# Kernel tuning notes

Hardware: AMD Instinct MI355X
Metric: run time of the kernel (lower is better)

The kernel has to match this reference:

```python
import jax, jax.numpy as jnp
import numpy as np

S, B, H = 2048, 32, 1024

def setup_inputs() -> dict:
    key = jax.random.key(0)
    k1, k2, k3, k4, k5 = jax.random.split(key, 5)
    stdv = 1.0 / np.sqrt(2 * H)  # nn.Linear default init scale (approx, uniform in torch)
    return {
        "hidden": jax.random.normal(k1, (1, B, H), dtype=jnp.float32),
        "encoder_outputs": jax.random.normal(k2, (S, B, H), dtype=jnp.float32),
        "W": jax.random.normal(k3, (H, 2 * H), dtype=jnp.float32) * stdv,
        "b": jax.random.normal(k4, (H,), dtype=jnp.float32) * stdv,
        "v": jax.random.normal(k5, (H,), dtype=jnp.float32) * (1.0 / np.sqrt(H)),
    }

def reference(hidden, encoder_outputs, W, b, v):
    # hidden: (1, B, H); encoder_outputs: (S, B, H)
    h = hidden[0]                              # (B, H)
    e = jnp.swapaxes(encoder_outputs, 0, 1)    # (B, S, H)
    Wh, We = W[:, :H], W[:, H:]                # split concat-linear: cat([H_rep, enc]) @ W^T
    # energy = tanh(Linear(cat([H, enc], -1)))  -> (B, S, H)
    pre_h = h @ Wh.T                           # (B, H), broadcast over S (H is repeated per step)
    pre_e = jnp.einsum('bsh,kh->bsk', e, We)   # (B, S, H)
    energy = jnp.tanh(pre_e + pre_h[:, None, :] + b)
    scores = jnp.einsum('bsk,k->bs', energy, v)  # v-dot per position -> (B, S)
    return jax.nn.softmax(scores, axis=1)[:, None, :]  # (B, 1, S)
```

## Files before the change

### kernel.cpp

```cpp
#include <hip/hip_runtime.h>


#define LDT 40

typedef __attribute__((ext_vector_type(8))) short short8;
typedef __attribute__((ext_vector_type(4))) float floatx4;
typedef __attribute__((ext_vector_type(4))) unsigned int uint4v;

#define GLDS(g, l) __builtin_amdgcn_global_load_lds( \
    (const __attribute__((address_space(1))) void*)(g), \
    (__attribute__((address_space(3))) void*)(l), 16, 0, 0)

__device__ __forceinline__ unsigned short f2b(float f) {
  union { float f; unsigned u; } c; c.f = f;
  unsigned r = c.u + 0x7fffu + ((c.u >> 16) & 1u);
  return (unsigned short)(r >> 16);
}

__device__ __forceinline__ unsigned pack2(float lo, float hi) {
  union { float f; unsigned u; } a, b; a.f = lo; b.f = hi;
  return __builtin_amdgcn_perm(b.u + 0x8000u, a.u + 0x8000u, 0x07060302u);
}

__device__ __forceinline__ float fast_tanh(float x) {
  float e = __expf(2.0f * x);
  return 1.0f - 2.0f / (e + 1.0f);
}

__global__ __launch_bounds__(256) void k_cvtB(
    const float* __restrict__ W, unsigned int* __restrict__ Bw) {
  const int idx = blockIdx.x * 256 + threadIdx.x;
  const int row = idx >> 8, col = (idx & 255) << 2;
  float4 f = *(const float4*)(W + (size_t)row * 2048 + 1024 + col);
  unsigned u0 = (unsigned)f2b(f.x) | ((unsigned)f2b(f.y) << 16);
  unsigned u1 = (unsigned)f2b(f.z) | ((unsigned)f2b(f.w) << 16);
  uint2 u = {u0, u1};
  *(uint2*)(Bw + ((size_t)row * 1024 + col) / 2) = u;
}

__global__ __launch_bounds__(256) void k_preh(
    const float* __restrict__ hidden, const float* __restrict__ W,
    const float* __restrict__ bias, float* __restrict__ tpre) {
  const int wv   = (blockIdx.x << 2) + (threadIdx.x >> 6);
  const int lane = threadIdx.x & 63;
  const int b = wv & 31;
  const int k = wv >> 5;
  const float* wr = W + (size_t)k * 2048;
  const float* hr = hidden + b * 1024;
  float s = 0.f;
  #pragma unroll
  for (int j = 0; j < 1024; j += 64) s += wr[j + lane] * hr[j + lane];
  #pragma unroll
  for (int off = 32; off; off >>= 1) s += __shfl_xor(s, off, 64);
  if (lane == 0) tpre[b * 1024 + k] = s + bias[k];
}

__global__ __launch_bounds__(256) void k_gemm(
    const float* __restrict__ A,
    const unsigned short* __restrict__ Bw,
    const float* __restrict__ tpre,
    const float* __restrict__ vvec,
    float* __restrict__ scoresT) {
  __shared__ short As[128 * LDT];
  __shared__ short Bs[128 * 32];

  const int l = blockIdx.x;
  const int x = l & 7, j = l >> 3;
  const int Mbase = (x * 64 + (j >> 3)) * 128;
  const int Nbase = (j & 7) * 128;

  const int tid = threadIdx.x, lane = tid & 63, w = tid >> 6;
  const int wm = w >> 1, wn = w & 1;
  const int c = lane & 15, q = lane >> 4;

  const float* ap = A + (size_t)(Mbase + (tid >> 1)) * 1024 + ((tid & 1) << 4);
  short* asw = &As[(tid >> 1) * LDT + ((tid & 1) << 4)];

  const unsigned short* bg0 =
      Bw + (size_t)(Nbase + w * 32 + (lane >> 2)) * 1024 + ((lane & 3) << 3);
  const unsigned short* bg1 = bg0 + (size_t)16 * 1024;
  short* bl0 = &Bs[(w * 32) * 32];
  short* bl1 = &Bs[(w * 32 + 16) * 32];

  floatx4 acc[4][4];
  #pragma unroll
  for (int mt = 0; mt < 4; ++mt)
    #pragma unroll
    for (int nt = 0; nt < 4; ++nt) {
      floatx4 z = {0.f, 0.f, 0.f, 0.f};
      acc[mt][nt] = z;
    }

  for (int k0 = 0; k0 < 1024; k0 += 32) {
    float4 f0 = *(const float4*)(ap + k0);
    float4 f1 = *(const float4*)(ap + k0 + 4);
    float4 f2 = *(const float4*)(ap + k0 + 8);
    float4 f3 = *(const float4*)(ap + k0 + 12);
    __syncthreads();
    GLDS(bg0 + k0, bl0);
    GLDS(bg1 + k0, bl1);
    uint4v u0 = {pack2(f0.x, f0.y), pack2(f0.z, f0.w),
                 pack2(f1.x, f1.y), pack2(f1.z, f1.w)};
    uint4v u1 = {pack2(f2.x, f2.y), pack2(f2.z, f2.w),
                 pack2(f3.x, f3.y), pack2(f3.z, f3.w)};
    *(uint4v*)asw = u0;
    *(uint4v*)(asw + 8) = u1;
    __syncthreads();

    short8 af[4], bf[4];
    #pragma unroll
    for (int mt = 0; mt < 4; ++mt)
      af[mt] = *(const short8*)&As[(wm * 64 + mt * 16 + c) * LDT + q * 8];
    #pragma unroll
    for (int nt = 0; nt < 4; ++nt)
      bf[nt] = *(const short8*)&Bs[(wn * 64 + nt * 16 + c) * 32 + q * 8];
    #pragma unroll
    for (int mt = 0; mt < 4; ++mt)
      #pragma unroll
      for (int nt = 0; nt < 4; ++nt)
        acc[mt][nt] = __builtin_amdgcn_mfma_f32_16x16x32_bf16(
            af[mt], bf[nt], acc[mt][nt], 0, 0, 0);
  }

  const int mwave = Mbase + wm * 64;
  const int nwave = Nbase + wn * 64;
  float vv[4];
  #pragma unroll
  for (int nt = 0; nt < 4; ++nt) vv[nt] = vvec[nwave + nt * 16 + c];
  #pragma unroll
  for (int mt = 0; mt < 4; ++mt) {
    #pragma unroll
    for (int i = 0; i < 4; ++i) {
      const int mrow = mwave + mt * 16 + q * 4 + i;
      const float* tb = tpre + (mrow & 31) * 1024;
      float ssum = 0.f;
      #pragma unroll
      for (int nt = 0; nt < 4; ++nt) {
        float pre = acc[mt][nt][i] + tb[nwave + nt * 16 + c];
        ssum += fast_tanh(pre) * vv[nt];
      }
      #pragma unroll
      for (int off = 1; off < 16; off <<= 1) ssum += __shfl_xor(ssum, off, 64);
      if (c == 0) atomicAdd(&scoresT[(mrow & 31) * 2048 + (mrow >> 5)], ssum);
    }
  }
}

__global__ __launch_bounds__(256) void k_softmax(
    const float* __restrict__ scoresT, float* __restrict__ out) {
  const int b = blockIdx.x;
  const int t = threadIdx.x;
  const int w = t >> 6, lane = t & 63;
  __shared__ float red[4];
  float vals[8];
  float m = -3.0e38f;
  #pragma unroll
  for (int i = 0; i < 8; ++i) {
    vals[i] = scoresT[b * 2048 + t + 256 * i];
    m = fmaxf(m, vals[i]);
  }
  #pragma unroll
  for (int off = 32; off; off >>= 1) m = fmaxf(m, __shfl_xor(m, off, 64));
  if (lane == 0) red[w] = m;
  __syncthreads();
  m = fmaxf(fmaxf(red[0], red[1]), fmaxf(red[2], red[3]));
  __syncthreads();
  float e[8];
  float sum = 0.f;
  #pragma unroll
  for (int i = 0; i < 8; ++i) { e[i] = __expf(vals[i] - m); sum += e[i]; }
  #pragma unroll
  for (int off = 32; off; off >>= 1) sum += __shfl_xor(sum, off, 64);
  if (lane == 0) red[w] = sum;
  __syncthreads();
  sum = red[0] + red[1] + red[2] + red[3];
  const float inv = 1.0f / sum;
  #pragma unroll
  for (int i = 0; i < 8; ++i) out[b * 2048 + t + 256 * i] = e[i] * inv;
}

extern "C" void kernel_launch(void* const* d_in, const int* in_sizes, int n_in,
                              void* d_out, int out_size, void* d_ws, size_t ws_size,
                              hipStream_t stream) {
  const float* hidden = (const float*)d_in[0];
  const float* enc    = (const float*)d_in[1];
  const float* W      = (const float*)d_in[2];
  const float* bias   = (const float*)d_in[3];
  const float* vvec   = (const float*)d_in[4];
  float* out = (float*)d_out;

  float* scoresT = (float*)d_ws;
  float* tpre    = scoresT + 65536;
  unsigned int* Bw = (unsigned int*)(tpre + 32768);

  hipMemsetAsync(scoresT, 0, 65536 * sizeof(float), stream);
  hipLaunchKernelGGL(k_cvtB, dim3(1024), dim3(256), 0, stream, W, Bw);
  hipLaunchKernelGGL(k_preh, dim3(8192), dim3(256), 0, stream, hidden, W, bias, tpre);
  hipLaunchKernelGGL(k_gemm, dim3(4096), dim3(256), 0, stream,
                     enc, (const unsigned short*)Bw, tpre, vvec, scoresT);
  hipLaunchKernelGGL(k_softmax, dim3(32), dim3(256), 0, stream, scoresT, out);
}
```

Baseline: 719.5 us.

## Double-buffer GEMM LDS tiles and fold score zeroing into conversion kernel

```diff
diff --git a/kernel.cpp b/kernel.cpp
--- a/kernel.cpp
+++ b/kernel.cpp
@@ -28,7 +28,8 @@
 }
 
 __global__ __launch_bounds__(256) void k_cvtB(
-    const float* __restrict__ W, unsigned int* __restrict__ Bw) {
+    const float* __restrict__ W, unsigned int* __restrict__ Bw,
+    float* __restrict__ scoresT) {
   const int idx = blockIdx.x * 256 + threadIdx.x;
   const int row = idx >> 8, col = (idx & 255) << 2;
   float4 f = *(const float4*)(W + (size_t)row * 2048 + 1024 + col);
@@ -36,6 +37,7 @@
   unsigned u1 = (unsigned)f2b(f.z) | ((unsigned)f2b(f.w) << 16);
   uint2 u = {u0, u1};
   *(uint2*)(Bw + ((size_t)row * 1024 + col) / 2) = u;
+  if (blockIdx.x < 256) scoresT[blockIdx.x * 256 + threadIdx.x] = 0.f;
 }
 
 __global__ __launch_bounds__(256) void k_preh(
@@ -61,8 +63,8 @@
     const float* __restrict__ tpre,
     const float* __restrict__ vvec,
     float* __restrict__ scoresT) {
-  __shared__ short As[128 * LDT];
-  __shared__ short Bs[128 * 32];
+  __shared__ short As[2][128 * LDT];
+  __shared__ short Bs[2][128 * 32];
 
   const int l = blockIdx.x;
   const int x = l & 7, j = l >> 3;
@@ -73,14 +75,14 @@
   const int wm = w >> 1, wn = w & 1;
   const int c = lane & 15, q = lane >> 4;
 
+  const int aoff = (tid >> 1) * LDT + ((tid & 1) << 4);
   const float* ap = A + (size_t)(Mbase + (tid >> 1)) * 1024 + ((tid & 1) << 4);
-  short* asw = &As[(tid >> 1) * LDT + ((tid & 1) << 4)];
 
   const unsigned short* bg0 =
       Bw + (size_t)(Nbase + w * 32 + (lane >> 2)) * 1024 + ((lane & 3) << 3);
   const unsigned short* bg1 = bg0 + (size_t)16 * 1024;
-  short* bl0 = &Bs[(w * 32) * 32];
-  short* bl1 = &Bs[(w * 32 + 16) * 32];
+  const int boff0 = (w * 32) * 32;
+  const int boff1 = (w * 32 + 16) * 32;
 
   floatx4 acc[4][4];
   #pragma unroll
@@ -91,35 +93,60 @@
       acc[mt][nt] = z;
     }
 
-  for (int k0 = 0; k0 < 1024; k0 += 32) {
-    float4 f0 = *(const float4*)(ap + k0);
-    float4 f1 = *(const float4*)(ap + k0 + 4);
-    float4 f2 = *(const float4*)(ap + k0 + 8);
-    float4 f3 = *(const float4*)(ap + k0 + 12);
-    __syncthreads();
-    GLDS(bg0 + k0, bl0);
-    GLDS(bg1 + k0, bl1);
+  {
+    float4 f0 = *(const float4*)(ap);
+    float4 f1 = *(const float4*)(ap + 4);
+    float4 f2 = *(const float4*)(ap + 8);
+    float4 f3 = *(const float4*)(ap + 12);
+    GLDS(bg0, &Bs[0][boff0]);
+    GLDS(bg1, &Bs[0][boff1]);
     uint4v u0 = {pack2(f0.x, f0.y), pack2(f0.z, f0.w),
                  pack2(f1.x, f1.y), pack2(f1.z, f1.w)};
     uint4v u1 = {pack2(f2.x, f2.y), pack2(f2.z, f2.w),
                  pack2(f3.x, f3.y), pack2(f3.z, f3.w)};
-    *(uint4v*)asw = u0;
-    *(uint4v*)(asw + 8) = u1;
-    __syncthreads();
+    *(uint4v*)&As[0][aoff] = u0;
+    *(uint4v*)&As[0][aoff + 8] = u1;
+  }
+  __syncthreads();
+
+  for (int k0 = 0; k0 < 1024; k0 += 32) {
+    const int cur = (k0 >> 5) & 1;
+    const int nxt = cur ^ 1;
+    const bool more = (k0 + 32) < 1024;
+
+    float4 g0, g1, g2, g3;
+    if (more) {
+      g0 = *(const float4*)(ap + k0 + 32);
+      g1 = *(const float4*)(ap + k0 + 36);
+      g2 = *(const float4*)(ap + k0 + 40);
+      g3 = *(const float4*)(ap + k0 + 44);
+      GLDS(bg0 + k0 + 32, &Bs[nxt][boff0]);
+      GLDS(bg1 + k0 + 32, &Bs[nxt][boff1]);
+    }
 
     short8 af[4], bf[4];
     #pragma unroll
     for (int mt = 0; mt < 4; ++mt)
-      af[mt] = *(const short8*)&As[(wm * 64 + mt * 16 + c) * LDT + q * 8];
+      af[mt] = *(const short8*)&As[cur][(wm * 64 + mt * 16 + c) * LDT + q * 8];
     #pragma unroll
     for (int nt = 0; nt < 4; ++nt)
-      bf[nt] = *(const short8*)&Bs[(wn * 64 + nt * 16 + c) * 32 + q * 8];
+      bf[nt] = *(const short8*)&Bs[cur][(wn * 64 + nt * 16 + c) * 32 + q * 8];
     #pragma unroll
     for (int mt = 0; mt < 4; ++mt)
       #pragma unroll
       for (int nt = 0; nt < 4; ++nt)
         acc[mt][nt] = __builtin_amdgcn_mfma_f32_16x16x32_bf16(
             af[mt], bf[nt], acc[mt][nt], 0, 0, 0);
+
+    if (more) {
+      uint4v u0 = {pack2(g0.x, g0.y), pack2(g0.z, g0.w),
+                   pack2(g1.x, g1.y), pack2(g1.z, g1.w)};
+      uint4v u1 = {pack2(g2.x, g2.y), pack2(g2.z, g2.w),
+                   pack2(g3.x, g3.y), pack2(g3.z, g3.w)};
+      *(uint4v*)&As[nxt][aoff] = u0;
+      *(uint4v*)&As[nxt][aoff + 8] = u1;
+    }
+    __syncthreads();
   }
 
   const int mwave = Mbase + wm * 64;
@@ -193,8 +220,7 @@
   float* tpre    = scoresT + 65536;
   unsigned int* Bw = (unsigned int*)(tpre + 32768);
 
-  hipMemsetAsync(scoresT, 0, 65536 * sizeof(float), stream);
-  hipLaunchKernelGGL(k_cvtB, dim3(1024), dim3(256), 0, stream, W, Bw);
+  hipLaunchKernelGGL(k_cvtB, dim3(1024), dim3(256), 0, stream, W, Bw, scoresT);
   hipLaunchKernelGGL(k_preh, dim3(8192), dim3(256), 0, stream, hidden, W, bias, tpre);
   hipLaunchKernelGGL(k_gemm, dim3(4096), dim3(256), 0, stream,
                      enc, (const unsigned short*)Bw, tpre, vvec, scoresT);
```

Result: slower. 744.8 us (+3.5%).

## Retile GEMM to 64x128 with K=64 steps and k-chunked B layout

Applied to the files above, without the earlier changes.

```diff
diff --git a/kernel.cpp b/kernel.cpp
--- a/kernel.cpp
+++ b/kernel.cpp
@@ -1,7 +1,7 @@
 #include <hip/hip_runtime.h>
 
 
-#define LDT 40
+#define LDA 72
 
 typedef __attribute__((ext_vector_type(8))) short short8;
 typedef __attribute__((ext_vector_type(4))) float floatx4;
@@ -28,107 +28,116 @@
 }
 
 __global__ __launch_bounds__(256) void k_cvtB(
-    const float* __restrict__ W, unsigned int* __restrict__ Bw) {
+    const float* __restrict__ W, unsigned int* __restrict__ Bw2,
+    float* __restrict__ scoresT) {
   const int idx = blockIdx.x * 256 + threadIdx.x;
-  const int row = idx >> 8, col = (idx & 255) << 2;
-  float4 f = *(const float4*)(W + (size_t)row * 2048 + 1024 + col);
-  unsigned u0 = (unsigned)f2b(f.x) | ((unsigned)f2b(f.y) << 16);
-  unsigned u1 = (unsigned)f2b(f.z) | ((unsigned)f2b(f.w) << 16);
-  uint2 u = {u0, u1};
-  *(uint2*)(Bw + ((size_t)row * 1024 + col) / 2) = u;
+  const int kc = idx >> 10, n = idx & 1023;
+  const float* src = W + (size_t)n * 2048 + 1024 + kc * 8;
+  float4 f0 = *(const float4*)(src);
+  float4 f1 = *(const float4*)(src + 4);
+  uint4v u = {pack2(f0.x, f0.y), pack2(f0.z, f0.w),
+              pack2(f1.x, f1.y), pack2(f1.z, f1.w)};
+  *(uint4v*)(Bw2 + ((size_t)kc * 8192 + n * 8) / 2) = u;
+  if (idx < 65536) scoresT[idx] = 0.f;
 }
 
 __global__ __launch_bounds__(256) void k_preh(
     const float* __restrict__ hidden, const float* __restrict__ W,
     const float* __restrict__ bias, float* __restrict__ tpre) {
-  const int wv   = (blockIdx.x << 2) + (threadIdx.x >> 6);
-  const int lane = threadIdx.x & 63;
-  const int b = wv & 31;
-  const int k = wv >> 5;
-  const float* wr = W + (size_t)k * 2048;
+  const int g  = blockIdx.x * 256 + threadIdx.x;
+  const int b  = g & 31;
+  const int ko = g >> 5;
+  const float* wr = W + (size_t)ko * 2048;
   const float* hr = hidden + b * 1024;
   float s = 0.f;
-  #pragma unroll
-  for (int j = 0; j < 1024; j += 64) s += wr[j + lane] * hr[j + lane];
-  #pragma unroll
-  for (int off = 32; off; off >>= 1) s += __shfl_xor(s, off, 64);
-  if (lane == 0) tpre[b * 1024 + k] = s + bias[k];
-}
-
-__global__ __launch_bounds__(256) void k_gemm(
+  #pragma unroll 8
+  for (int j = 0; j < 1024; j += 4) {
+    float4 wv = *(const float4*)(wr + j);
+    float4 hv = *(const float4*)(hr + j);
+    s += wv.x * hv.x + wv.y * hv.y + wv.z * hv.z + wv.w * hv.w;
+  }
+  tpre[b * 1024 + ko] = s + bias[ko];
+}
+
+__global__ __launch_bounds__(256, 4) void k_gemm(
     const float* __restrict__ A,
-    const unsigned short* __restrict__ Bw,
+    const unsigned short* __restrict__ Bw2,
     const float* __restrict__ tpre,
     const float* __restrict__ vvec,
     float* __restrict__ scoresT) {
-  __shared__ short As[128 * LDT];
-  __shared__ short Bs[128 * 32];
+  __shared__ short As[64 * LDA];
+  __shared__ short Bs[8 * 128 * 8];
 
   const int l = blockIdx.x;
   const int x = l & 7, j = l >> 3;
-  const int Mbase = (x * 64 + (j >> 3)) * 128;
+  const int Mbase = (x * 128 + (j >> 3)) * 64;
   const int Nbase = (j & 7) * 128;
 
   const int tid = threadIdx.x, lane = tid & 63, w = tid >> 6;
   const int wm = w >> 1, wn = w & 1;
   const int c = lane & 15, q = lane >> 4;
 
-  const float* ap = A + (size_t)(Mbase + (tid >> 1)) * 1024 + ((tid & 1) << 4);
-  short* asw = &As[(tid >> 1) * LDT + ((tid & 1) << 4)];
-
-  const unsigned short* bg0 =
-      Bw + (size_t)(Nbase + w * 32 + (lane >> 2)) * 1024 + ((lane & 3) << 3);
-  const unsigned short* bg1 = bg0 + (size_t)16 * 1024;
-  short* bl0 = &Bs[(w * 32) * 32];
-  short* bl1 = &Bs[(w * 32 + 16) * 32];
-
-  floatx4 acc[4][4];
-  #pragma unroll
-  for (int mt = 0; mt < 4; ++mt)
+  const int arow = tid >> 2, acol = (tid & 3) << 4;
+  const float* ap = A + (size_t)(Mbase + arow) * 1024 + acol;
+  short* asw = &As[arow * LDA + acol];
+
+  const unsigned short* bgb = Bw2 + (size_t)(Nbase + lane) * 8;
+
+  floatx4 acc[2][4];
+  #pragma unroll
+  for (int mt = 0; mt < 2; ++mt)
     #pragma unroll
     for (int nt = 0; nt < 4; ++nt) {
       floatx4 z = {0.f, 0.f, 0.f, 0.f};
       acc[mt][nt] = z;
     }
 
-  for (int k0 = 0; k0 < 1024; k0 += 32) {
-    float4 f0 = *(const float4*)(ap + k0);
-    float4 f1 = *(const float4*)(ap + k0 + 4);
-    float4 f2 = *(const float4*)(ap + k0 + 8);
-    float4 f3 = *(const float4*)(ap + k0 + 12);
-    __syncthreads();
-    GLDS(bg0 + k0, bl0);
-    GLDS(bg1 + k0, bl1);
-    uint4v u0 = {pack2(f0.x, f0.y), pack2(f0.z, f0.w),
-                 pack2(f1.x, f1.y), pack2(f1.z, f1.w)};
-    uint4v u1 = {pack2(f2.x, f2.y), pack2(f2.z, f2.w),
-                 pack2(f3.x, f3.y), pack2(f3.z, f3.w)};
+  for (int k0 = 0; k0 < 1024; k0 += 64) {
+    float4 g0 = *(const float4*)(ap + k0);
+    float4 g1 = *(const float4*)(ap + k0 + 4);
+    float4 g2 = *(const float4*)(ap + k0 + 8);
+    float4 g3 = *(const float4*)(ap + k0 + 12);
+    #pragma unroll
+    for (int i = 0; i < 4; ++i) {
+      const int seg = w * 4 + i;
+      const int kcl = seg >> 1, half = seg & 1;
+      GLDS(bgb + ((size_t)((k0 >> 3) + kcl) * 8192 + half * 512),
+           &Bs[kcl * 1024 + half * 512]);
+    }
+    uint4v u0 = {pack2(g0.x, g0.y), pack2(g0.z, g0.w),
+                 pack2(g1.x, g1.y), pack2(g1.z, g1.w)};
+    uint4v u1 = {pack2(g2.x, g2.y), pack2(g2.z, g2.w),
+                 pack2(g3.x, g3.y), pack2(g3.z, g3.w)};
     *(uint4v*)asw = u0;
     *(uint4v*)(asw + 8) = u1;
     __syncthreads();
 
-    short8 af[4], bf[4];
-    #pragma unroll
-    for (int mt = 0; mt < 4; ++mt)
-      af[mt] = *(const short8*)&As[(wm * 64 + mt * 16 + c) * LDT + q * 8];
-    #pragma unroll
-    for (int nt = 0; nt < 4; ++nt)
-      bf[nt] = *(const short8*)&Bs[(wn * 64 + nt * 16 + c) * 32 + q * 8];
-    #pragma unroll
-    for (int mt = 0; mt < 4; ++mt)
+    #pragma unroll
+    for (int ks = 0; ks < 2; ++ks) {
+      short8 af[2], bf[4];
+      #pragma unroll
+      for (int mt = 0; mt < 2; ++mt)
+        af[mt] = *(const short8*)&As[(wm * 32 + mt * 16 + c) * LDA + ks * 32 + q * 8];
       #pragma unroll
       for (int nt = 0; nt < 4; ++nt)
-        acc[mt][nt] = __builtin_amdgcn_mfma_f32_16x16x32_bf16(
-            af[mt], bf[nt], acc[mt][nt], 0, 0, 0);
-  }
-
-  const int mwave = Mbase + wm * 64;
+        bf[nt] = *(const short8*)&Bs[(ks * 4 + q) * 1024 + (wn * 64 + nt * 16 + c) * 8];
+      #pragma unroll
+      for (int mt = 0; mt < 2; ++mt)
+        #pragma unroll
+        for (int nt = 0; nt < 4; ++nt)
+          acc[mt][nt] = __builtin_amdgcn_mfma_f32_16x16x32_bf16(
+              af[mt], bf[nt], acc[mt][nt], 0, 0, 0);
+    }
+    __syncthreads();
+  }
+
+  const int mwave = Mbase + wm * 32;
   const int nwave = Nbase + wn * 64;
   float vv[4];
   #pragma unroll
   for (int nt = 0; nt < 4; ++nt) vv[nt] = vvec[nwave + nt * 16 + c];
   #pragma unroll
-  for (int mt = 0; mt < 4; ++mt) {
+  for (int mt = 0; mt < 2; ++mt) {
     #pragma unroll
     for (int i = 0; i < 4; ++i) {
       const int mrow = mwave + mt * 16 + q * 4 + i;
@@ -191,12 +200,11 @@
 
   float* scoresT = (float*)d_ws;
   float* tpre    = scoresT + 65536;
-  unsigned int* Bw = (unsigned int*)(tpre + 32768);
-
-  hipMemsetAsync(scoresT, 0, 65536 * sizeof(float), stream);
-  hipLaunchKernelGGL(k_cvtB, dim3(1024), dim3(256), 0, stream, W, Bw);
-  hipLaunchKernelGGL(k_preh, dim3(8192), dim3(256), 0, stream, hidden, W, bias, tpre);
-  hipLaunchKernelGGL(k_gemm, dim3(4096), dim3(256), 0, stream,
-                     enc, (const unsigned short*)Bw, tpre, vvec, scoresT);
+  unsigned int* Bw2 = (unsigned int*)(tpre + 32768);
+
+  hipLaunchKernelGGL(k_cvtB, dim3(512), dim3(256), 0, stream, W, Bw2, scoresT);
+  hipLaunchKernelGGL(k_preh, dim3(128), dim3(256), 0, stream, hidden, W, bias, tpre);
+  hipLaunchKernelGGL(k_gemm, dim3(8192), dim3(256), 0, stream,
+                     enc, (const unsigned short*)Bw2, tpre, vvec, scoresT);
   hipLaunchKernelGGL(k_softmax, dim3(32), dim3(256), 0, stream, scoresT, out);
 }
```

After: 597.0 us. 1.21x faster.
